# Kernel tuning notes

Hardware: AMD Instinct MI355X
Metric: run time of the kernel (lower is better)

The kernel has to match this reference:

```python
import jax, jax.numpy as jnp
import numpy as np

N, E = 50000, 800000
D_IN, HID, HEADS, D_OUT = 128, 32, 4, 40
NEG_SLOPE = 0.2
BN_EPS = 1e-5


def gat_conv(x, src, dst, W, a_src, a_dst, b, heads, ch):
    """PyG-style GATConv (eval mode, self-loops already appended to src/dst)."""
    n = x.shape[0]
    h = (x @ W).reshape(n, heads, ch)                      # [N,H,C]
    al_src = jnp.einsum('nhc,hc->nh', h, a_src)            # [N,H]
    al_dst = jnp.einsum('nhc,hc->nh', h, a_dst)
    e = jax.nn.leaky_relu(al_src[src] + al_dst[dst], NEG_SLOPE)  # [Etot,H]
    # segment softmax over incoming edges of each dst node
    e_max = jax.ops.segment_max(e, dst, num_segments=n)
    e = jnp.exp(e - e_max[dst])
    denom = jax.ops.segment_sum(e, dst, num_segments=n)
    alpha = e / (denom[dst] + 1e-16)                        # [Etot,H]
    msg = h[src] * alpha[:, :, None]                        # [Etot,H,C]
    out = jax.ops.segment_sum(msg, dst, num_segments=n)     # [N,H,C]
    return out.reshape(n, heads * ch) + b


def bn_eval(x, g, b, m, v):
    return (x - m) * jax.lax.rsqrt(v + BN_EPS) * g + b


def setup_inputs() -> dict:
    key = jax.random.key(0)
    ks = jax.random.split(key, 24)
    p = lambda k, s: jax.random.normal(k, s, jnp.float32) * 0.1
    inp = {
        'x': jax.random.normal(ks[0], (N, D_IN), jnp.float32),
        'edge_index': jax.random.randint(ks[1], (2, E), 0, N),
        'W1': p(ks[2], (D_IN, HEADS * HID)),
        'a_src1': p(ks[3], (HEADS, HID)), 'a_dst1': p(ks[4], (HEADS, HID)),
        'b1': jnp.zeros((HEADS * HID,), jnp.float32),
        'W2': p(ks[5], (HEADS * HID, HEADS * HID)),
        'a_src2': p(ks[6], (HEADS, HID)), 'a_dst2': p(ks[7], (HEADS, HID)),
        'b2': jnp.zeros((HEADS * HID,), jnp.float32),
        'W3': p(ks[8], (HEADS * HID, D_OUT)),
        'a_src3': p(ks[9], (1, D_OUT)), 'a_dst3': p(ks[10], (1, D_OUT)),
        'b3': jnp.zeros((D_OUT,), jnp.float32),
        'bn1_g': jnp.ones((HEADS * HID,), jnp.float32),
        'bn1_b': jnp.zeros((HEADS * HID,), jnp.float32),
        'bn1_m': p(ks[11], (HEADS * HID,)),
        'bn1_v': jax.random.uniform(ks[12], (HEADS * HID,), jnp.float32) + 0.5,
        'bn2_g': jnp.ones((HEADS * HID,), jnp.float32),
        'bn2_b': jnp.zeros((HEADS * HID,), jnp.float32),
        'bn2_m': p(ks[13], (HEADS * HID,)),
        'bn2_v': jax.random.uniform(ks[14], (HEADS * HID,), jnp.float32) + 0.5,
    }
    return inp


def reference(x, edge_index, W1, a_src1, a_dst1, b1, W2, a_src2, a_dst2, b2,
              W3, a_src3, a_dst3, b3, bn1_g, bn1_b, bn1_m, bn1_v,
              bn2_g, bn2_b, bn2_m, bn2_v):
    n = x.shape[0]
    loop = jnp.arange(n, dtype=edge_index.dtype)
    src = jnp.concatenate([edge_index[0], loop])   # add self loops (PyG default)
    dst = jnp.concatenate([edge_index[1], loop])

    h = gat_conv(x, src, dst, W1, a_src1, a_dst1, b1, HEADS, HID)
    h = jax.nn.relu(h)
    h = bn_eval(h, bn1_g, bn1_b, bn1_m, bn1_v)      # dropout = identity (eval)

    h = gat_conv(h, src, dst, W2, a_src2, a_dst2, b2, HEADS, HID)
    h = jax.nn.relu(h)
    h = bn_eval(h, bn2_g, bn2_b, bn2_m, bn2_v)

    h = gat_conv(h, src, dst, W3, a_src3, a_dst3, b3, 1, D_OUT)
    return jax.nn.log_softmax(h, axis=1)
```

## Files before the change

kernel.cpp:

```cpp
#include <hip/hip_runtime.h>
#include <hip/hip_bf16.h>
#include <math.h>

using bf16 = __hip_bfloat16;
using frag8 = __attribute__((ext_vector_type(8))) short;
using f32x4 = __attribute__((ext_vector_type(4))) float;

#define LEAKY 0.2f
#define BN_EPS 1e-5f
#define NEGBIG -1e30f
#define BSHIFT 9

__device__ __forceinline__ float lrelu(float z){ return fmaxf(z, LEAKY * z); }
__device__ __forceinline__ float bflo(unsigned u){ return __uint_as_float(u << 16); }
__device__ __forceinline__ float bfhi(unsigned u){ return __uint_as_float(u & 0xffff0000u); }
__device__ __forceinline__ unsigned pk(float a, float b){
  unsigned ua = __float_as_uint(a), ub = __float_as_uint(b);
  ua += 0x7fffu + ((ua >> 16) & 1u);
  ub += 0x7fffu + ((ub >> 16) & 1u);
  return (ua >> 16) | (ub & 0xffff0000u);
}
__device__ __forceinline__ float ldf(const void* p, size_t i, int isbf){
  if (isbf) return (float)((const bf16*)p)[i];
  return ((const float*)p)[i];
}

union U4F8 { uint4 u; frag8 f; };

__device__ __forceinline__ frag8 load_a_pairs(const unsigned* __restrict__ X2, int node, int k0){
  U4F8 v; v.u = *((const uint4*)(X2 + (size_t)node*64 + (k0 >> 1))); return v.f;
}
__device__ __forceinline__ frag8 load_a_f32(const float* __restrict__ X, int node, int k0){
  float4 q0 = *((const float4*)(X + (size_t)node*128 + k0));
  float4 q1 = *((const float4*)(X + (size_t)node*128 + k0 + 4));
  U4F8 v; v.u = make_uint4(pk(q0.x,q0.y), pk(q0.z,q0.w), pk(q1.x,q1.y), pk(q1.z,q1.w));
  return v.f;
}

__global__ void init_detect(int* cnt, int* bcnt, const unsigned short* __restrict__ w1bits,
                            int* flag, int* total, int n){
  int g = blockIdx.x*256 + threadIdx.x;
  if (g < n) cnt[g] = 0;
  if (g < 256) bcnt[g] = 0;
  if (g == 0) *total = 0;
  if (blockIdx.x == 0){
    __shared__ int cntr;
    if (threadIdx.x == 0) cntr = 0;
    __syncthreads();
    unsigned u = w1bits[threadIdx.x * 2];
    int e = (u >> 7) & 0xff;
    atomicAdd(&cntr, (e >= 64 && e <= 140) ? 1 : 0);
    __syncthreads();
    if (threadIdx.x == 0) *flag = (cntr >= 160) ? 1 : 0;
  }
}

__global__ __launch_bounds__(256) void hist(const int* __restrict__ dst, int* cnt,
                                            int* bcnt, int e, int n){
  __shared__ int lb[256];
  const int t = threadIdx.x;
  lb[t] = 0;
  __syncthreads();
  const int c0 = blockIdx.x*4096;
  const int lim = min(4096, e - c0);
  for (int i = t; i < lim; i += 256){
    int d = dst[c0 + i];
    if ((unsigned)d < (unsigned)n){
      atomicAdd(&cnt[d], 1);
      atomicAdd(&lb[min(d >> BSHIFT, 255)], 1);
    }
  }
  __syncthreads();
  if (lb[t]) atomicAdd(&bcnt[t], lb[t]);
}

__global__ void csr_scan(const int* __restrict__ cnt, int* start, int* pos,
                         int* total, int n){
  __shared__ int s[256];
  __shared__ int base_s;
  int t = threadIdx.x;
  int g = blockIdx.x*256 + t;
  int v = (g < n) ? cnt[g] : 0;
  s[t] = v;
  __syncthreads();
  for (int off = 1; off < 256; off <<= 1){
    int x = (t >= off) ? s[t-off] : 0;
    __syncthreads();
    s[t] += x;
    __syncthreads();
  }
  if (t == 255) base_s = atomicAdd(total, s[255]);
  __syncthreads();
  if (g < n){
    int st = base_s + s[t] - v;
    start[g] = st;
    pos[g] = st;
  }
}

__global__ void bscan(const int* __restrict__ bcnt, int* bstart, int* bpos){
  __shared__ int s[256];
  int t = threadIdx.x;
  int v = bcnt[t];
  s[t] = v;
  __syncthreads();
  for (int off = 1; off < 256; off <<= 1){
    int x = (t >= off) ? s[t-off] : 0;
    __syncthreads();
    s[t] += x;
    __syncthreads();
  }
  int st = s[t] - v;
  bstart[t] = st;
  bpos[t] = st;
}

__global__ __launch_bounds__(256) void bsort(const int* __restrict__ src,
                                             const int* __restrict__ dst,
                                             int* bpos, int2* __restrict__ ebuf,
                                             int e, int n){
  __shared__ int lh[256], lo[256], gb[256];
  __shared__ int tot_s;
  __shared__ int2 buf[4096];
  const int t = threadIdx.x;
  const int c0 = blockIdx.x*4096;
  if (c0 >= e) return;
  const int lim = min(4096, e - c0);
  lh[t] = 0;
  __syncthreads();
  int2 ev[16]; int bk[16];
  #pragma unroll
  for (int j = 0; j < 16; ++j){
    const int i = j*256 + t;
    const bool valid = i < lim;
    int s = 0, d = 0;
    if (valid){ s = src[c0 + i]; d = dst[c0 + i]; }
    ev[j] = make_int2(s, d);
    bk[j] = (valid && (unsigned)d < (unsigned)n) ? min(d >> BSHIFT, 255) : -1;
    if (bk[j] >= 0) atomicAdd(&lh[bk[j]], 1);
  }
  __syncthreads();
  const int v = lh[t];
  lo[t] = v;
  __syncthreads();
  for (int off = 1; off < 256; off <<= 1){
    int x = (t >= off) ? lo[t-off] : 0;
    __syncthreads();
    lo[t] += x;
    __syncthreads();
  }
  if (t == 255) tot_s = lo[255];
  lo[t] -= v;
  if (v) gb[t] = atomicAdd(&bpos[t], v);
  lh[t] = 0;
  __syncthreads();
  #pragma unroll
  for (int j = 0; j < 16; ++j){
    if (bk[j] >= 0){
      int r = atomicAdd(&lh[bk[j]], 1);
      buf[lo[bk[j]] + r] = ev[j];
    }
  }
  __syncthreads();
  const int tot = tot_s;
  for (int i = t; i < tot; i += 256){
    int2 sd = buf[i];
    int b = min(sd.y >> BSHIFT, 255);
    ebuf[gb[b] + (i - lo[b])] = sd;
  }
}

__global__ __launch_bounds__(512) void cscat(const int2* __restrict__ ebuf,
                                             const int* __restrict__ bstart,
                                             const int* __restrict__ bpos,
                                             int* pos, int* __restrict__ col){
  const int b = blockIdx.x;
  const int s1 = bpos[b];
  for (int i = bstart[b] + threadIdx.x; i < s1; i += 512){
    int2 sd = ebuf[i];
    int p = atomicAdd(&pos[sd.y], 1);
    col[p] = sd.x;
  }
}

__global__ __launch_bounds__(256) void gemm_al_mfma(
    const void* __restrict__ X, int xkind,
    const void* __restrict__ W, const void* __restrict__ Wsrc, const void* __restrict__ Wdst,
    const int* __restrict__ flagp,
    unsigned* __restrict__ H2, float* __restrict__ AL, float* __restrict__ AD,
    int n, int ntiles)
{
  __shared__ unsigned short WT[128*136];
  const int isbf = *flagp;
  const int t = threadIdx.x;
  if (isbf){
    const unsigned short* W16 = (const unsigned short*)W;
    for (int idx = t; idx < 16384; idx += 256){
      int k = idx >> 7, nn = idx & 127;
      WT[nn*136 + k] = W16[idx];
    }
  } else {
    const float* Wf = (const float*)W;
    for (int idx = t; idx < 16384; idx += 256){
      int k = idx >> 7, nn = idx & 127;
      WT[nn*136 + k] = (unsigned short)(pk(Wf[idx], 0.f) & 0xffffu);
    }
  }
  __syncthreads();
  const int w = t >> 6;
  const int lane = t & 63;
  const int m = lane & 15, quad = lane >> 4;

  frag8 bf[4][2];
  #pragma unroll
  for (int s = 0; s < 4; ++s)
    #pragma unroll
    for (int ct = 0; ct < 2; ++ct){
      int colc = w*32 + ct*16 + m;
      int k0 = s*32 + quad*8;
      U4F8 v; v.u = *((const uint4*)&WT[colc*136 + k0]);
      bf[s][ct] = v.f;
    }
  float avv[2], dvv[2];
  #pragma unroll
  for (int ct = 0; ct < 2; ++ct){
    int colc = w*32 + ct*16 + m;
    avv[ct] = ldf(Wsrc, colc, isbf);
    dvv[ct] = ldf(Wdst, colc, isbf);
  }
  const bool pairs = (xkind == 1) || isbf;

  for (int tile = blockIdx.x; tile < ntiles; tile += gridDim.x){
    const int mb = tile*16;
    int nodeA = mb + m; if (nodeA >= n) nodeA = n - 1;
    frag8 af[4];
    #pragma unroll
    for (int s = 0; s < 4; ++s){
      int k0 = s*32 + quad*8;
      af[s] = pairs ? load_a_pairs((const unsigned*)X, nodeA, k0)
                    : load_a_f32((const float*)X, nodeA, k0);
    }
    f32x4 acc0 = {0.f,0.f,0.f,0.f}, acc1 = {0.f,0.f,0.f,0.f};
    #pragma unroll
    for (int s = 0; s < 4; ++s){
      acc0 = __builtin_amdgcn_mfma_f32_16x16x32_bf16(af[s], bf[s][0], acc0, 0,0,0);
      acc1 = __builtin_amdgcn_mfma_f32_16x16x32_bf16(af[s], bf[s][1], acc1, 0,0,0);
    }
    #pragma unroll
    for (int r = 0; r < 4; ++r){
      int g = mb + quad*4 + r;
      float v0 = acc0[r], v1 = acc1[r];
      unsigned u0 = pk(v0, __shfl_xor(v0, 1));
      unsigned u1 = pk(v1, __shfl_xor(v1, 1));
      bool ok = g < n;
      if (((lane & 1) == 0) && ok){
        H2[(size_t)g*64 + w*16 + (m >> 1)]     = u0;
        H2[(size_t)g*64 + w*16 + 8 + (m >> 1)] = u1;
      }
      float s1 = v0*avv[0] + v1*avv[1];
      float s2 = v0*dvv[0] + v1*dvv[1];
      s1 += __shfl_xor(s1,1); s1 += __shfl_xor(s1,2); s1 += __shfl_xor(s1,4); s1 += __shfl_xor(s1,8);
      s2 += __shfl_xor(s2,1); s2 += __shfl_xor(s2,2); s2 += __shfl_xor(s2,4); s2 += __shfl_xor(s2,8);
      if (m == 0 && ok){ AL[g*4 + w] = s1; AD[g*4 + w] = s2; }
    }
  }
}

__global__ __launch_bounds__(256) void gemm3_mfma(
    const unsigned* __restrict__ X2, const void* __restrict__ W,
    const void* __restrict__ Wsrc, const void* __restrict__ Wdst,
    const int* __restrict__ flagp,
    unsigned* __restrict__ H3, float* __restrict__ AL, float* __restrict__ AD,
    int n, int ntiles)
{
  __shared__ unsigned short WT[48*136];
  const int isbf = *flagp;
  const int t = threadIdx.x;
  for (int idx = t; idx < 128*64; idx += 256){
    int c = idx & 63, k = idx >> 6;
    if (c < 48){
      unsigned short v = 0;
      if (c < 40){
        if (isbf) v = ((const unsigned short*)W)[k*40 + c];
        else      v = (unsigned short)(pk(((const float*)W)[k*40 + c], 0.f) & 0xffffu);
      }
      WT[c*136 + k] = v;
    }
  }
  __syncthreads();
  const int w = t >> 6;
  const int lane = t & 63;
  const int m = lane & 15, quad = lane >> 4;

  frag8 bf[4][3];
  float avv[3], dvv[3];
  #pragma unroll
  for (int ct = 0; ct < 3; ++ct){
    int colc = ct*16 + m;
    #pragma unroll
    for (int s = 0; s < 4; ++s){
      int k0 = s*32 + quad*8;
      U4F8 v; v.u = *((const uint4*)&WT[colc*136 + k0]);
      bf[s][ct] = v.f;
    }
    avv[ct] = (colc < 40) ? ldf(Wsrc, colc, isbf) : 0.f;
    dvv[ct] = (colc < 40) ? ldf(Wdst, colc, isbf) : 0.f;
  }

  for (int tg = blockIdx.x; tg*4 < ntiles; tg += gridDim.x){
    const int tile = tg*4 + w;
    if (tile >= ntiles) continue;
    const int mb = tile*16;
    int nodeA = mb + m; if (nodeA >= n) nodeA = n - 1;
    frag8 af[4];
    #pragma unroll
    for (int s = 0; s < 4; ++s)
      af[s] = load_a_pairs(X2, nodeA, s*32 + quad*8);
    f32x4 acc[3];
    #pragma unroll
    for (int ct = 0; ct < 3; ++ct) acc[ct] = (f32x4){0.f,0.f,0.f,0.f};
    #pragma unroll
    for (int s = 0; s < 4; ++s){
      acc[0] = __builtin_amdgcn_mfma_f32_16x16x32_bf16(af[s], bf[s][0], acc[0], 0,0,0);
      acc[1] = __builtin_amdgcn_mfma_f32_16x16x32_bf16(af[s], bf[s][1], acc[1], 0,0,0);
      acc[2] = __builtin_amdgcn_mfma_f32_16x16x32_bf16(af[s], bf[s][2], acc[2], 0,0,0);
    }
    #pragma unroll
    for (int r = 0; r < 4; ++r){
      int g = mb + quad*4 + r;
      bool ok = g < n;
      float ps = 0.f, pd = 0.f;
      #pragma unroll
      for (int ct = 0; ct < 3; ++ct){
        float v = acc[ct][r];
        ps += v*avv[ct]; pd += v*dvv[ct];
        unsigned u = pk(v, __shfl_xor(v, 1));
        bool stok = ((lane & 1) == 0) && ok && (ct < 2 || m < 8);
        if (stok) H3[(size_t)g*20 + ct*8 + (m >> 1)] = u;
      }
      ps += __shfl_xor(ps,1); ps += __shfl_xor(ps,2); ps += __shfl_xor(ps,4); ps += __shfl_xor(ps,8);
      pd += __shfl_xor(pd,1); pd += __shfl_xor(pd,2); pd += __shfl_xor(pd,4); pd += __shfl_xor(pd,8);
      if (m == 0 && ok){ AL[g] = ps; AD[g] = pd; }
    }
  }
}

__global__ __launch_bounds__(256) void agg4(
    const unsigned* __restrict__ H2,
    const float* __restrict__ ALf, const float* __restrict__ ADf,
    const int* __restrict__ cnt, const int* __restrict__ start, const int* __restrict__ col,
    const void* __restrict__ bias, const void* __restrict__ bng, const void* __restrict__ bnb,
    const void* __restrict__ bnm,  const void* __restrict__ bnv,
    const int* __restrict__ flagp,
    unsigned* __restrict__ Hout, int n)
{
  const int isbf = *flagp;
  const int wave = threadIdx.x >> 6;
  const int lane = threadIdx.x & 63;
  const int node = blockIdx.x*4 + wave;
  if (node >= n) return;
  const int head = lane >> 4;
  const float ad = ADf[node*4 + head];
  const int base = start[node], deg = cnt[node];

  float accL, accH, l;
  {
    float e = __expf(lrelu(ALf[node*4 + head] + ad));
    unsigned h = H2[(size_t)node*64 + lane];
    l = e; accL = e * bflo(h); accH = e * bfhi(h);
  }

  int i = 0;
  for (; i + 8 <= deg; i += 8){
    int sv[8]; float av[8]; unsigned hv[8];
    #pragma unroll
    for (int u = 0; u < 8; ++u){
      int s = col[base + i + u];
      sv[u] = ((unsigned)s < (unsigned)n) ? s : 0;
    }
    #pragma unroll
    for (int u = 0; u < 8; ++u) av[u] = ALf[sv[u]*4 + head];
    #pragma unroll
    for (int u = 0; u < 8; ++u) hv[u] = H2[(size_t)sv[u]*64 + lane];
    #pragma unroll
    for (int u = 0; u < 8; ++u){
      float e = __expf(lrelu(av[u] + ad));
      l    += e;
      accL += e * bflo(hv[u]);
      accH += e * bfhi(hv[u]);
    }
  }
  for (; i < deg; ++i){
    int s = col[base + i];
    if ((unsigned)s >= (unsigned)n) s = 0;
    float a = ALf[s*4 + head];
    unsigned h = H2[(size_t)s*64 + lane];
    float e = __expf(lrelu(a + ad));
    l += e; accL += e * bflo(h); accH += e * bfhi(h);
  }

  const float rl = 1.f / l;
  const int c0 = 2*lane, c1 = c0 + 1;
  float v0 = fmaxf(accL*rl + ldf(bias,c0,isbf), 0.f);
  v0 = (v0 - ldf(bnm,c0,isbf)) * rsqrtf(ldf(bnv,c0,isbf) + BN_EPS) * ldf(bng,c0,isbf) + ldf(bnb,c0,isbf);
  float v1 = fmaxf(accH*rl + ldf(bias,c1,isbf), 0.f);
  v1 = (v1 - ldf(bnm,c1,isbf)) * rsqrtf(ldf(bnv,c1,isbf) + BN_EPS) * ldf(bng,c1,isbf) + ldf(bnb,c1,isbf);
  Hout[(size_t)node*64 + lane] = pk(v0, v1);
}

__global__ __launch_bounds__(256) void agg1(
    const unsigned* __restrict__ H3,
    const float* __restrict__ AL, const float* __restrict__ AD,
    const int* __restrict__ cnt, const int* __restrict__ start, const int* __restrict__ col,
    const void* __restrict__ b3, const int* __restrict__ flagp,
    void* __restrict__ out, int n)
{
  const int isbf = *flagp;
  const int wave = threadIdx.x >> 6;
  const int lane = threadIdx.x & 63;
  const int node = blockIdx.x*4 + wave;
  if (node >= n) return;
  const float ad = AD[node];
  const bool act = lane < 20;
  const int base = start[node], deg = cnt[node];

  float accL, accH, l;
  {
    float e = __expf(lrelu(AL[node] + ad));
    unsigned h = act ? H3[(size_t)node*20 + lane] : 0u;
    l = e; accL = e * bflo(h); accH = e * bfhi(h);
  }

  int i = 0;
  for (; i + 8 <= deg; i += 8){
    int sv[8]; float av[8]; unsigned hv[8];
    #pragma unroll
    for (int u = 0; u < 8; ++u){
      int s = col[base + i + u];
      sv[u] = ((unsigned)s < (unsigned)n) ? s : 0;
    }
    #pragma unroll
    for (int u = 0; u < 8; ++u) av[u] = AL[sv[u]];
    #pragma unroll
    for (int u = 0; u < 8; ++u) hv[u] = act ? H3[(size_t)sv[u]*20 + lane] : 0u;
    #pragma unroll
    for (int u = 0; u < 8; ++u){
      float e = __expf(lrelu(av[u] + ad));
      l    += e;
      accL += e * bflo(hv[u]);
      accH += e * bfhi(hv[u]);
    }
  }
  for (; i < deg; ++i){
    int s = col[base + i];
    if ((unsigned)s >= (unsigned)n) s = 0;
    float a = AL[s];
    unsigned h = act ? H3[(size_t)s*20 + lane] : 0u;
    float e = __expf(lrelu(a + ad));
    l += e; accL += e * bflo(h); accH += e * bfhi(h);
  }

  const float rl = 1.f / l;
  const int c0 = 2*lane;
  float z0 = act ? (accL*rl + ldf(b3, c0,     isbf)) : NEGBIG;
  float z1 = act ? (accH*rl + ldf(b3, c0 + 1, isbf)) : NEGBIG;
  float mx = fmaxf(z0, z1);
  #pragma unroll
  for (int off = 1; off < 64; off <<= 1) mx = fmaxf(mx, __shfl_xor(mx, off));
  float p = act ? (__expf(z0 - mx) + __expf(z1 - mx)) : 0.f;
  float sum = p;
  #pragma unroll
  for (int off = 1; off < 64; off <<= 1) sum += __shfl_xor(sum, off);
  if (act){
    float lg = __logf(sum);
    float r0 = z0 - mx - lg, r1 = z1 - mx - lg;
    if (isbf) ((unsigned*)out)[(size_t)node*20 + lane] = pk(r0, r1);
    else      ((float2*)out)[(size_t)node*20 + lane] = make_float2(r0, r1);
  }
}

extern "C" void kernel_launch(void* const* d_in, const int* in_sizes, int n_in,
                              void* d_out, int out_size, void* d_ws, size_t ws_size,
                              hipStream_t stream)
{
  (void)n_in; (void)out_size; (void)ws_size;
  const void* x    = d_in[0];
  const int*  ei   = (const int*)d_in[1];
  const void* W1   = d_in[2];
  const void* as1  = d_in[3];
  const void* ad1  = d_in[4];
  const void* b1   = d_in[5];
  const void* W2   = d_in[6];
  const void* as2  = d_in[7];
  const void* ad2  = d_in[8];
  const void* b2   = d_in[9];
  const void* W3   = d_in[10];
  const void* as3  = d_in[11];
  const void* ad3  = d_in[12];
  const void* b3   = d_in[13];
  const void* bn1g = d_in[14];
  const void* bn1b = d_in[15];
  const void* bn1m = d_in[16];
  const void* bn1v = d_in[17];
  const void* bn2g = d_in[18];
  const void* bn2b = d_in[19];
  const void* bn2m = d_in[20];
  const void* bn2v = d_in[21];

  const int N  = in_sizes[0] / 128;
  const int E  = in_sizes[1] / 2;
  const int ntiles = (N + 15) / 16;

  char* w = (char*)d_ws;
  size_t off = 0;
  auto alloc = [&](size_t bytes)->char*{
    char* p = w + off; off = (off + bytes + 255) & ~(size_t)255; return p;
  };
  unsigned* H2A = (unsigned*)alloc((size_t)N*64*4);
  unsigned* H2B = (unsigned*)alloc((size_t)N*64*4);
  unsigned* H3p = (unsigned*)alloc((size_t)N*20*4);
  float* AL   = (float*)alloc((size_t)N*4*4);
  float* AD   = (float*)alloc((size_t)N*4*4);
  int*   cnt   = (int*)alloc((size_t)N*4);
  int*   start = (int*)alloc((size_t)N*4);
  int*   pos   = (int*)alloc((size_t)N*4);
  int*   col   = (int*)alloc((size_t)E*4);
  int2*  ebuf  = (int2*)alloc((size_t)E*8);
  int*   bcnt  = (int*)alloc(1024);
  int*   bstart= (int*)alloc(1024);
  int*   bpos  = (int*)alloc(1024);
  int*   flag  = (int*)alloc(256);
  int*   total = (int*)alloc(256);

  const int* srcp = ei;
  const int* dstp = ei + E;

  const int nb256 = (N + 255)/256;
  const int nbCH = (E + 4095)/4096;
  const int bb = (N + 3)/4;
  int g1 = ntiles < 625 ? ntiles : 625;
  int g3 = (ntiles + 3)/4; if (g3 > 400) g3 = 400;

  init_detect<<<nb256,256,0,stream>>>(cnt, bcnt, (const unsigned short*)W1, flag, total, N);
  hist<<<nbCH,256,0,stream>>>(dstp, cnt, bcnt, E, N);
  csr_scan<<<nb256,256,0,stream>>>(cnt, start, pos, total, N);
  bscan<<<1,256,0,stream>>>(bcnt, bstart, bpos);
  bsort<<<nbCH,256,0,stream>>>(srcp, dstp, bpos, ebuf, E, N);
  cscat<<<256,512,0,stream>>>(ebuf, bstart, bpos, pos, col);

  gemm_al_mfma<<<g1,256,0,stream>>>(x, 0, W1, as1, ad1, flag, H2A, AL, AD, N, ntiles);
  agg4<<<bb,256,0,stream>>>(H2A, AL, AD, cnt, start, col,
                            b1, bn1g, bn1b, bn1m, bn1v, flag, H2B, N);
  gemm_al_mfma<<<g1,256,0,stream>>>(H2B, 1, W2, as2, ad2, flag, H2A, AL, AD, N, ntiles);
  agg4<<<bb,256,0,stream>>>(H2A, AL, AD, cnt, start, col,
                            b2, bn2g, bn2b, bn2m, bn2v, flag, H2B, N);
  gemm3_mfma<<<g3,256,0,stream>>>(H2B, W3, as3, ad3, flag, H3p, AL, AD, N, ntiles);
  agg1<<<bb,256,0,stream>>>(H3p, AL, AD, cnt, start, col, b3, flag, d_out, N);
}
```

Measured before the change: 397.0 us.

## Build CSR per bucket in LDS and share edge softmax weights via shuffles

Removes the global per-node degree atomics in hist and the separate csr_scan kernel. A new bfinal kernel computes per-node degrees, prefix offsets and column placement inside LDS for each 512-node bucket, replacing global atomics on pos. In the aggregation kernels, each lane computes one edge/head attention exponent and broadcasts it with shuffles, instead of every lane redundantly loading AL and computing exp for all 8 edges. This cuts redundant loads and exps but adds shuffle latency, and bfinal assumes bucket count NB matches the 256-bucket layout, which holds here since N/512 is under 256.

Result: faster. 353.0 us (-11.1%).

```diff
diff --git a/kernel.cpp b/kernel.cpp
--- a/kernel.cpp
+++ b/kernel.cpp
@@ -37,25 +37,20 @@
   return v.f;
 }
 
-__global__ void init_detect(int* cnt, int* bcnt, const unsigned short* __restrict__ w1bits,
-                            int* flag, int* total, int n){
-  int g = blockIdx.x*256 + threadIdx.x;
-  if (g < n) cnt[g] = 0;
-  if (g < 256) bcnt[g] = 0;
-  if (g == 0) *total = 0;
-  if (blockIdx.x == 0){
-    __shared__ int cntr;
-    if (threadIdx.x == 0) cntr = 0;
-    __syncthreads();
-    unsigned u = w1bits[threadIdx.x * 2];
-    int e = (u >> 7) & 0xff;
-    atomicAdd(&cntr, (e >= 64 && e <= 140) ? 1 : 0);
-    __syncthreads();
-    if (threadIdx.x == 0) *flag = (cntr >= 160) ? 1 : 0;
-  }
-}
-
-__global__ __launch_bounds__(256) void hist(const int* __restrict__ dst, int* cnt,
+__global__ void init_detect(int* bcnt, const unsigned short* __restrict__ w1bits,
+                            int* flag){
+  __shared__ int cntr;
+  if (threadIdx.x == 0) cntr = 0;
+  bcnt[threadIdx.x] = 0;
+  __syncthreads();
+  unsigned u = w1bits[threadIdx.x * 2];
+  int e = (u >> 7) & 0xff;
+  atomicAdd(&cntr, (e >= 64 && e <= 140) ? 1 : 0);
+  __syncthreads();
+  if (threadIdx.x == 0) *flag = (cntr >= 160) ? 1 : 0;
+}
+
+__global__ __launch_bounds__(256) void hist(const int* __restrict__ dst,
                                             int* bcnt, int e, int n){
   __shared__ int lb[256];
   const int t = threadIdx.x;
@@ -65,37 +60,11 @@
   const int lim = min(4096, e - c0);
   for (int i = t; i < lim; i += 256){
     int d = dst[c0 + i];
-    if ((unsigned)d < (unsigned)n){
-      atomicAdd(&cnt[d], 1);
+    if ((unsigned)d < (unsigned)n)
       atomicAdd(&lb[min(d >> BSHIFT, 255)], 1);
-    }
   }
   __syncthreads();
   if (lb[t]) atomicAdd(&bcnt[t], lb[t]);
-}
-
-__global__ void csr_scan(const int* __restrict__ cnt, int* start, int* pos,
-                         int* total, int n){
-  __shared__ int s[256];
-  __shared__ int base_s;
-  int t = threadIdx.x;
-  int g = blockIdx.x*256 + t;
-  int v = (g < n) ? cnt[g] : 0;
-  s[t] = v;
-  __syncthreads();
-  for (int off = 1; off < 256; off <<= 1){
-    int x = (t >= off) ? s[t-off] : 0;
-    __syncthreads();
-    s[t] += x;
-    __syncthreads();
-  }
-  if (t == 255) base_s = atomicAdd(total, s[255]);
-  __syncthreads();
-  if (g < n){
-    int st = base_s + s[t] - v;
-    start[g] = st;
-    pos[g] = st;
-  }
 }
 
 __global__ void bscan(const int* __restrict__ bcnt, int* bstart, int* bpos){
@@ -170,16 +139,41 @@
   }
 }
 
-__global__ __launch_bounds__(512) void cscat(const int2* __restrict__ ebuf,
-                                             const int* __restrict__ bstart,
-                                             const int* __restrict__ bpos,
-                                             int* pos, int* __restrict__ col){
-  const int b = blockIdx.x;
-  const int s1 = bpos[b];
-  for (int i = bstart[b] + threadIdx.x; i < s1; i += 512){
+__global__ __launch_bounds__(256) void bfinal(const int2* __restrict__ ebuf,
+    const int* __restrict__ bstart, const int* __restrict__ bpos,
+    int* __restrict__ cnt, int* __restrict__ start, int* __restrict__ col, int n){
+  __shared__ int deg[512], off[512], ps[256];
+  const int b = blockIdx.x, t = threadIdx.x;
+  const int n0 = b << BSHIFT;
+  const int e0 = bstart[b], e1 = bpos[b];
+  deg[t] = 0; deg[t + 256] = 0;
+  __syncthreads();
+  for (int i = e0 + t; i < e1; i += 256)
+    atomicAdd(&deg[ebuf[i].y - n0], 1);
+  __syncthreads();
+  int p = deg[2*t] + deg[2*t + 1];
+  ps[t] = p;
+  __syncthreads();
+  for (int o = 1; o < 256; o <<= 1){
+    int x = (t >= o) ? ps[t - o] : 0;
+    __syncthreads();
+    ps[t] += x;
+    __syncthreads();
+  }
+  int ex = ps[t] - p;
+  off[2*t]     = ex;
+  off[2*t + 1] = ex + deg[2*t];
+  __syncthreads();
+  #pragma unroll
+  for (int j = t; j < 512; j += 256){
+    int node = n0 + j;
+    if (node < n){ cnt[node] = deg[j]; start[node] = e0 + off[j]; }
+  }
+  __syncthreads();
+  for (int i = e0 + t; i < e1; i += 256){
     int2 sd = ebuf[i];
-    int p = atomicAdd(&pos[sd.y], 1);
-    col[p] = sd.x;
+    int r = atomicAdd(&off[sd.y - n0], 1);
+    col[e0 + r] = sd.x;
   }
 }
 
@@ -361,6 +355,9 @@
   if (node >= n) return;
   const int head = lane >> 4;
   const float ad = ADf[node*4 + head];
+  const int eu = (lane >> 2) & 7;
+  const int eh = lane & 3;
+  const float ade = ADf[node*4 + eh];
   const int base = start[node], deg = cnt[node];
 
   float accL, accH, l;
@@ -372,22 +369,22 @@
 
   int i = 0;
   for (; i + 8 <= deg; i += 8){
-    int sv[8]; float av[8]; unsigned hv[8];
+    int sv[8]; unsigned hv[8];
     #pragma unroll
     for (int u = 0; u < 8; ++u){
       int s = col[base + i + u];
       sv[u] = ((unsigned)s < (unsigned)n) ? s : 0;
     }
-    #pragma unroll
-    for (int u = 0; u < 8; ++u) av[u] = ALf[sv[u]*4 + head];
+    float ave = ALf[sv[eu]*4 + eh];
     #pragma unroll
     for (int u = 0; u < 8; ++u) hv[u] = H2[(size_t)sv[u]*64 + lane];
+    float ew = __expf(lrelu(ave + ade));
     #pragma unroll
     for (int u = 0; u < 8; ++u){
-      float e = __expf(lrelu(av[u] + ad));
+      float e = __shfl(ew, (u << 2) + head);
       l    += e;
-      accL += e * bflo(hv[u]);
-      accH += e * bfhi(hv[u]);
+      accL = fmaf(e, bflo(hv[u]), accL);
+      accH = fmaf(e, bfhi(hv[u]), accH);
     }
   }
   for (; i < deg; ++i){
@@ -422,6 +419,7 @@
   if (node >= n) return;
   const float ad = AD[node];
   const bool act = lane < 20;
+  const int eu = lane & 7;
   const int base = start[node], deg = cnt[node];
 
   float accL, accH, l;
@@ -433,22 +431,22 @@
 
   int i = 0;
   for (; i + 8 <= deg; i += 8){
-    int sv[8]; float av[8]; unsigned hv[8];
+    int sv[8]; unsigned hv[8];
     #pragma unroll
     for (int u = 0; u < 8; ++u){
       int s = col[base + i + u];
       sv[u] = ((unsigned)s < (unsigned)n) ? s : 0;
     }
-    #pragma unroll
-    for (int u = 0; u < 8; ++u) av[u] = AL[sv[u]];
+    float ave = AL[sv[eu]];
     #pragma unroll
     for (int u = 0; u < 8; ++u) hv[u] = act ? H3[(size_t)sv[u]*20 + lane] : 0u;
+    float ew = __expf(lrelu(ave + ad));
     #pragma unroll
     for (int u = 0; u < 8; ++u){
-      float e = __expf(lrelu(av[u] + ad));
+      float e = __shfl(ew, u);
       l    += e;
-      accL += e * bflo(hv[u]);
-      accH += e * bfhi(hv[u]);
+      accL = fmaf(e, bflo(hv[u]), accL);
+      accH = fmaf(e, bfhi(hv[u]), accH);
     }
   }
   for (; i < deg; ++i){
@@ -523,30 +521,27 @@
   float* AD   = (float*)alloc((size_t)N*4*4);
   int*   cnt   = (int*)alloc((size_t)N*4);
   int*   start = (int*)alloc((size_t)N*4);
-  int*   pos   = (int*)alloc((size_t)N*4);
   int*   col   = (int*)alloc((size_t)E*4);
   int2*  ebuf  = (int2*)alloc((size_t)E*8);
   int*   bcnt  = (int*)alloc(1024);
   int*   bstart= (int*)alloc(1024);
   int*   bpos  = (int*)alloc(1024);
   int*   flag  = (int*)alloc(256);
-  int*   total = (int*)alloc(256);
 
   const int* srcp = ei;
   const int* dstp = ei + E;
 
-  const int nb256 = (N + 255)/256;
   const int nbCH = (E + 4095)/4096;
+  const int NB = (N + 511) >> BSHIFT;
   const int bb = (N + 3)/4;
   int g1 = ntiles < 625 ? ntiles : 625;
   int g3 = (ntiles + 3)/4; if (g3 > 400) g3 = 400;
 
-  init_detect<<<nb256,256,0,stream>>>(cnt, bcnt, (const unsigned short*)W1, flag, total, N);
-  hist<<<nbCH,256,0,stream>>>(dstp, cnt, bcnt, E, N);
-  csr_scan<<<nb256,256,0,stream>>>(cnt, start, pos, total, N);
+  init_detect<<<1,256,0,stream>>>(bcnt, (const unsigned short*)W1, flag);
+  hist<<<nbCH,256,0,stream>>>(dstp, bcnt, E, N);
   bscan<<<1,256,0,stream>>>(bcnt, bstart, bpos);
   bsort<<<nbCH,256,0,stream>>>(srcp, dstp, bpos, ebuf, E, N);
-  cscat<<<256,512,0,stream>>>(ebuf, bstart, bpos, pos, col);
+  bfinal<<<NB,256,0,stream>>>(ebuf, bstart, bpos, cnt, start, col, N);
 
   gemm_al_mfma<<<g1,256,0,stream>>>(x, 0, W1, as1, ad1, flag, H2A, AL, AD, N, ntiles);
   agg4<<<bb,256,0,stream>>>(H2A, AL, AD, cnt, start, col,
```
